# Performance work log

Measured on AMD Instinct MI355X. Metric: run time of the kernel, lower is better.

Reference implementation:

```python
import jax, jax.numpy as jnp
import numpy as np

GT_POSITIVE_THRESHOLD = 3.0  # pixels, from config['gt_positive_threshold']


def setup_inputs() -> dict:
    key = jax.random.key(0)
    k0, k1, k2 = jax.random.split(key, 3)
    B, N0, N1 = 8, 2048, 2048
    W, H = 640.0, 480.0
    scale = jnp.array([W, H], dtype=jnp.float32)
    kpts0 = jax.random.uniform(k0, (B, N0, 2), dtype=jnp.float32) * scale
    kpts1 = jax.random.uniform(k1, (B, N1, 2), dtype=jnp.float32) * scale
    # near-identity homography per pair (small perturbation keeps points in-frame)
    transformation = (jnp.eye(3, dtype=jnp.float32)[None]
                      + 0.001 * jax.random.normal(k2, (B, 3, 3), dtype=jnp.float32))
    return {"kpts0": kpts0, "kpts1": kpts1, "transformation": transformation}


def _reproject_keypoints(kpts, H):
    # kpts: [B,N,2], H: [B,3,3] homography. Homogeneous projection.
    ones = jnp.ones(kpts.shape[:-1] + (1,), dtype=kpts.dtype)
    pts_h = jnp.concatenate([kpts, ones], axis=-1)           # [B,N,3]
    proj = jnp.einsum('bij,bnj->bni', H, pts_h)              # [B,N,3]
    return proj[..., :2] / (proj[..., 2:3] + 1e-8)


def _cdist(a, b):
    # a: [B,N0,2], b: [B,N1,2] -> [B,N0,N1] Euclidean distances
    a2 = jnp.sum(a * a, axis=-1)                             # [B,N0]
    b2 = jnp.sum(b * b, axis=-1)                             # [B,N1]
    ab = jnp.einsum('bnd,bmd->bnm', a, b)                    # [B,N0,N1]
    d2 = a2[:, :, None] + b2[:, None, :] - 2.0 * ab
    return jnp.sqrt(jnp.maximum(d2, 0.0))


def reference(kpts0, kpts1, transformation):
    B, N0, _ = kpts0.shape
    N1 = kpts1.shape[1]
    kpts0_t = _reproject_keypoints(kpts0, transformation)
    err = _cdist(kpts0_t, kpts1)                             # [B,N0,N1]

    min_dist0 = jnp.min(err, axis=2)                         # [B,N0]
    gt_matches0 = jnp.argmin(err, axis=2).astype(jnp.int32)  # [B,N0]
    gt_matches1 = jnp.argmin(err, axis=1).astype(jnp.int32)  # [B,N1]

    # cross-check: kpts1's best match of kpts0's best match must be the kpt itself
    back = jnp.take_along_axis(gt_matches1, gt_matches0, axis=1)  # [B,N0]
    idx0 = jnp.arange(N0, dtype=jnp.int32)[None, :]
    inconsistent = (back != idx0) | (min_dist0 > GT_POSITIVE_THRESHOLD)
    gt_matches0 = jnp.where(inconsistent, -1, gt_matches0)

    # rebuild inverse map: gt_matches1[b, gt_matches0[b,i]] = i for valid i
    valid = gt_matches0 != -1
    tgt = jnp.where(valid, gt_matches0, N1)                  # N1 is out-of-range -> dropped
    src = jnp.broadcast_to(idx0, (B, N0))
    gt_matches1_out = jnp.full((B, N1), -1, dtype=jnp.int32)
    gt_matches1_out = gt_matches1_out.at[jnp.arange(B)[:, None], tgt].set(src, mode='drop')

    return gt_matches0, gt_matches1_out, min_dist0
```

## Files before the change

### kernel.cpp

```cpp
#include <hip/hip_runtime.h>


#define SPN 2048
#define SPT 16384

__device__ __forceinline__ void sp_reproject(const float* __restrict__ T, int b,
                                             float x, float y,
                                             float& X, float& Y, float& S) {
  const float* H = T + b * 9;
  float p0 = __fadd_rn(__fadd_rn(__fmul_rn(H[0], x), __fmul_rn(H[1], y)), H[2]);
  float p1 = __fadd_rn(__fadd_rn(__fmul_rn(H[3], x), __fmul_rn(H[4], y)), H[5]);
  float p2 = __fadd_rn(__fadd_rn(__fmul_rn(H[6], x), __fmul_rn(H[7], y)), H[8]);
  float den = __fadd_rn(p2, 1e-8f);
  X = __fdiv_rn(p0, den);
  Y = __fdiv_rn(p1, den);
  S = __fadd_rn(__fmul_rn(X, X), __fmul_rn(Y, Y));
}

__global__ __launch_bounds__(256) void sp_prep(
    const float2* __restrict__ k0, const float2* __restrict__ k1,
    const float* __restrict__ T, float4* __restrict__ q0, float4* __restrict__ q1) {
  int t = blockIdx.x * 256 + threadIdx.x;
  if (t < SPT) {
    float2 p = k0[t];
    float X, Y, S;
    sp_reproject(T, t >> 11, p.x, p.y, X, Y, S);
    q0[t] = make_float4(X, Y, S, 0.0f);
  } else {
    int u = t - SPT;
    float2 p = k1[u];
    float S = __fadd_rn(__fmul_rn(p.x, p.x), __fmul_rn(p.y, p.y));
    q1[u] = make_float4(p.x, p.y, S, 0.0f);
  }
}

__device__ __forceinline__ void sp_row8(
    const float rx[8], const float ry[8], const float rs[8],
    float bv[8], int bi[8], float4 v, int c) {
#pragma unroll
  for (int r = 0; r < 8; r++) {
    float ab = __fadd_rn(__fmul_rn(rx[r], v.x), __fmul_rn(ry[r], v.y));
    float d2 = __fsub_rn(__fadd_rn(rs[r], v.z), __fmul_rn(2.0f, ab));
    float dm = fmaxf(d2, 0.0f);
    if (dm < bv[r]) { bv[r] = dm; bi[r] = c; }
  }
}

__global__ __launch_bounds__(256, 4) void SuperPointMatchesGenerator_56925496541369_kernel(
    const float4* __restrict__ q0, const float4* __restrict__ q1,
    unsigned short* __restrict__ gt0p, unsigned short* __restrict__ gt1,
    float* __restrict__ out_mind) {
  const bool m1 = blockIdx.x >= SPN;
  const int base = (m1 ? blockIdx.x - SPN : blockIdx.x) * 8;
  const int b = base >> 11, cb = b << 11;
  const float4* __restrict__ qr = m1 ? q1 : q0;
  const float4* __restrict__ qc = (m1 ? q0 : q1) + cb;

  float rx[8], ry[8], rs[8], bv[8];
  int bi[8];
#pragma unroll
  for (int r = 0; r < 8; r++) {
    float4 v = qr[base + r];
    rx[r] = v.x; ry[r] = v.y; rs[r] = v.z;
    bv[r] = INFINITY; bi[r] = 0;
  }

#pragma unroll 1
  for (int c = threadIdx.x; c < SPN; c += 512) {
    float4 va = qc[c];
    float4 vb = qc[c + 256];
    sp_row8(rx, ry, rs, bv, bi, va, c);
    sp_row8(rx, ry, rs, bv, bi, vb, c + 256);
  }

  unsigned long long key[8];
#pragma unroll
  for (int r = 0; r < 8; r++)
    key[r] = ((unsigned long long)__float_as_uint(bv[r]) << 32) | (unsigned)bi[r];
#pragma unroll
  for (int off = 32; off > 0; off >>= 1) {
#pragma unroll
    for (int r = 0; r < 8; r++) {
      unsigned long long o = __shfl_down(key[r], off);
      if (o < key[r]) key[r] = o;
    }
  }
  __shared__ unsigned long long part[4][8];
  if ((threadIdx.x & 63) == 0) {
    int w = threadIdx.x >> 6;
#pragma unroll
    for (int r = 0; r < 8; r++) part[w][r] = key[r];
  }
  __syncthreads();
  if (threadIdx.x < 8) {
    int r = threadIdx.x;
    unsigned long long k = part[0][r];
#pragma unroll
    for (int w = 1; w < 4; w++)
      if (part[w][r] < k) k = part[w][r];
    int idx = (int)(k & 0x7ffu);
    if (!m1) {
      float e = __fsqrt_rn(__uint_as_float((unsigned)(k >> 32)));
      unsigned short pk = (unsigned short)idx;
      if (e > 3.0f) pk |= 0x8000u;
      gt0p[base + r] = pk;
      out_mind[base + r] = e;
    } else {
      gt1[base + r] = (unsigned short)idx;
    }
  }
}

__global__ __launch_bounds__(256) void SuperPointMatchesGenerator_56925496541369_final(
    const unsigned short* __restrict__ gt0p, const unsigned short* __restrict__ gt1,
    float* __restrict__ out) {
  int t = blockIdx.x * 256 + threadIdx.x;
  if (t >= SPT) return;
  int b = t >> 11, i = t & 2047, cb = b << 11;

  unsigned short p0 = gt0p[t];
  int m0 = p0 & 0x7ff;
  bool ok0 = ((p0 & 0x8000u) == 0) && ((int)gt1[cb + m0] == i);
  out[t] = ok0 ? (float)m0 : -1.0f;

  int istar = gt1[t];
  unsigned short ps = gt0p[cb + istar];
  bool ok1 = (((int)(ps & 0x7ff)) == i) && ((ps & 0x8000u) == 0);
  out[SPT + t] = ok1 ? (float)istar : -1.0f;
}

__global__ __launch_bounds__(256) void sp_fb_main(
    const float2* __restrict__ k0, const float2* __restrict__ k1,
    const float* __restrict__ T, unsigned short* __restrict__ gt0p,
    unsigned short* __restrict__ gt1, float* __restrict__ out_mind) {
  const bool mode1 = blockIdx.x >= SPN;
  const int base = (mode1 ? blockIdx.x - SPN : blockIdx.x) * 8;
  const int b = base >> 11, cb = b << 11;
  float rx[8], ry[8], rs[8], bv[8];
  int bi[8];
#pragma unroll
  for (int r = 0; r < 8; r++) { bv[r] = INFINITY; bi[r] = 0; }
  if (!mode1) {
#pragma unroll
    for (int r = 0; r < 8; r++) {
      float2 p = k0[base + r];
      sp_reproject(T, b, p.x, p.y, rx[r], ry[r], rs[r]);
    }
    for (int c = threadIdx.x; c < SPN; c += 256) {
      float2 p = k1[cb + c];
      float b2 = __fadd_rn(__fmul_rn(p.x, p.x), __fmul_rn(p.y, p.y));
#pragma unroll
      for (int r = 0; r < 8; r++) {
        float ab = __fadd_rn(__fmul_rn(rx[r], p.x), __fmul_rn(ry[r], p.y));
        float d2 = __fsub_rn(__fadd_rn(rs[r], b2), __fmul_rn(2.0f, ab));
        float dm = fmaxf(d2, 0.0f);
        if (dm < bv[r]) { bv[r] = dm; bi[r] = c; }
      }
    }
  } else {
#pragma unroll
    for (int r = 0; r < 8; r++) {
      float2 p = k1[base + r];
      rx[r] = p.x; ry[r] = p.y;
      rs[r] = __fadd_rn(__fmul_rn(p.x, p.x), __fmul_rn(p.y, p.y));
    }
    for (int c = threadIdx.x; c < SPN; c += 256) {
      float2 p = k0[cb + c];
      float cx, cy, a2;
      sp_reproject(T, b, p.x, p.y, cx, cy, a2);
#pragma unroll
      for (int r = 0; r < 8; r++) {
        float ab = __fadd_rn(__fmul_rn(rx[r], cx), __fmul_rn(ry[r], cy));
        float d2 = __fsub_rn(__fadd_rn(a2, rs[r]), __fmul_rn(2.0f, ab));
        float dm = fmaxf(d2, 0.0f);
        if (dm < bv[r]) { bv[r] = dm; bi[r] = c; }
      }
    }
  }
  unsigned long long key[8];
#pragma unroll
  for (int r = 0; r < 8; r++)
    key[r] = ((unsigned long long)__float_as_uint(bv[r]) << 32) | (unsigned)bi[r];
#pragma unroll
  for (int off = 32; off > 0; off >>= 1) {
#pragma unroll
    for (int r = 0; r < 8; r++) {
      unsigned long long o = __shfl_down(key[r], off);
      if (o < key[r]) key[r] = o;
    }
  }
  __shared__ unsigned long long part[4][8];
  if ((threadIdx.x & 63) == 0) {
    int w = threadIdx.x >> 6;
#pragma unroll
    for (int r = 0; r < 8; r++) part[w][r] = key[r];
  }
  __syncthreads();
  if (threadIdx.x < 8) {
    int r = threadIdx.x;
    unsigned long long k = part[0][r];
#pragma unroll
    for (int w = 1; w < 4; w++)
      if (part[w][r] < k) k = part[w][r];
    int idx = (int)(k & 0x7ffu);
    if (!mode1) {
      float e = __fsqrt_rn(__uint_as_float((unsigned)(k >> 32)));
      unsigned short pk = (unsigned short)idx;
      if (e > 3.0f) pk |= 0x8000u;
      gt0p[base + r] = pk;
      out_mind[base + r] = e;
    } else {
      gt1[base + r] = (unsigned short)idx;
    }
  }
}

extern "C" void kernel_launch(void* const* d_in, const int* in_sizes, int n_in,
                              void* d_out, int out_size, void* d_ws, size_t ws_size,
                              hipStream_t stream) {
  (void)in_sizes; (void)n_in; (void)out_size;
  const float2* k0 = (const float2*)d_in[0];
  const float2* k1 = (const float2*)d_in[1];
  const float* T   = (const float*)d_in[2];
  float* out = (float*)d_out;

  const size_t need = (size_t)2 * SPT * sizeof(float4) + (size_t)2 * SPT * sizeof(unsigned short);
  if (ws_size >= need) {
    float4* q0 = (float4*)d_ws;
    float4* q1 = q0 + SPT;
    unsigned short* gt0p = (unsigned short*)(q1 + SPT);
    unsigned short* gt1  = gt0p + SPT;
    sp_prep<<<2 * SPT / 256, 256, 0, stream>>>(k0, k1, T, q0, q1);
    SuperPointMatchesGenerator_56925496541369_kernel<<<2 * SPN, 256, 0, stream>>>(
        q0, q1, gt0p, gt1, out + 2 * SPT);
    SuperPointMatchesGenerator_56925496541369_final<<<SPT / 256, 256, 0, stream>>>(
        gt0p, gt1, out);
  } else {
    unsigned short* gt0p = (unsigned short*)d_ws;
    unsigned short* gt1  = gt0p + SPT;
    sp_fb_main<<<2 * SPN, 256, 0, stream>>>(k0, k1, T, gt0p, gt1, out + 2 * SPT);
    SuperPointMatchesGenerator_56925496541369_final<<<SPT / 256, 256, 0, stream>>>(
        gt0p, gt1, out);
  }
}
```

Measured before the change: 82.36 us.

## Stage candidates in LDS, process 16 rows per block, reduce via shared memory

Each block now loads the batch's 2048 candidate points into a 32KB shared-memory tile and tracks 16 rows per thread instead of 8, halving the block count. The clamp to zero moves after the loop, and the doubled row coordinates are precomputed to shave arithmetic per pair. The final argmin reduction goes through shared memory, with each wave finishing four rows. This trades extra LDS use and register pressure (lower occupancy) for less global traffic and more reuse per candidate load.

```diff
diff --git a/kernel.cpp b/kernel.cpp
--- a/kernel.cpp
+++ b/kernel.cpp
@@ -34,79 +34,84 @@
   }
 }
 
-__device__ __forceinline__ void sp_row8(
-    const float rx[8], const float ry[8], const float rs[8],
-    float bv[8], int bi[8], float4 v, int c) {
-#pragma unroll
-  for (int r = 0; r < 8; r++) {
-    float ab = __fadd_rn(__fmul_rn(rx[r], v.x), __fmul_rn(ry[r], v.y));
-    float d2 = __fsub_rn(__fadd_rn(rs[r], v.z), __fmul_rn(2.0f, ab));
-    float dm = fmaxf(d2, 0.0f);
-    if (dm < bv[r]) { bv[r] = dm; bi[r] = c; }
-  }
-}
-
 __global__ __launch_bounds__(256, 4) void SuperPointMatchesGenerator_56925496541369_kernel(
     const float4* __restrict__ q0, const float4* __restrict__ q1,
     unsigned short* __restrict__ gt0p, unsigned short* __restrict__ gt1,
     float* __restrict__ out_mind) {
-  const bool m1 = blockIdx.x >= SPN;
-  const int base = (m1 ? blockIdx.x - SPN : blockIdx.x) * 8;
+  __shared__ float4 cand[SPN];
+  const int tid = threadIdx.x;
+  const bool m1 = blockIdx.x >= (SPT / 16);
+  const int base = (m1 ? blockIdx.x - (SPT / 16) : blockIdx.x) << 4;
   const int b = base >> 11, cb = b << 11;
   const float4* __restrict__ qr = m1 ? q1 : q0;
   const float4* __restrict__ qc = (m1 ? q0 : q1) + cb;
 
-  float rx[8], ry[8], rs[8], bv[8];
-  int bi[8];
-#pragma unroll
-  for (int r = 0; r < 8; r++) {
+  float4 stage[8];
+#pragma unroll
+  for (int k = 0; k < 8; k++) stage[k] = qc[(k << 8) + tid];
+#pragma unroll
+  for (int k = 0; k < 8; k++) cand[(k << 8) + tid] = stage[k];
+
+  float rx2[16], ry2[16], rsv[16], bv[16];
+  int bi[16];
+#pragma unroll
+  for (int r = 0; r < 16; r++) {
     float4 v = qr[base + r];
-    rx[r] = v.x; ry[r] = v.y; rs[r] = v.z;
+    rx2[r] = __fmul_rn(2.0f, v.x);
+    ry2[r] = __fmul_rn(2.0f, v.y);
+    rsv[r] = v.z;
     bv[r] = INFINITY; bi[r] = 0;
   }
-
-#pragma unroll 1
-  for (int c = threadIdx.x; c < SPN; c += 512) {
-    float4 va = qc[c];
-    float4 vb = qc[c + 256];
-    sp_row8(rx, ry, rs, bv, bi, va, c);
-    sp_row8(rx, ry, rs, bv, bi, vb, c + 256);
-  }
-
-  unsigned long long key[8];
-#pragma unroll
-  for (int r = 0; r < 8; r++)
-    key[r] = ((unsigned long long)__float_as_uint(bv[r]) << 32) | (unsigned)bi[r];
-#pragma unroll
-  for (int off = 32; off > 0; off >>= 1) {
-#pragma unroll
-    for (int r = 0; r < 8; r++) {
-      unsigned long long o = __shfl_down(key[r], off);
-      if (o < key[r]) key[r] = o;
-    }
-  }
-  __shared__ unsigned long long part[4][8];
-  if ((threadIdx.x & 63) == 0) {
-    int w = threadIdx.x >> 6;
-#pragma unroll
-    for (int r = 0; r < 8; r++) part[w][r] = key[r];
-  }
-  __syncthreads();
-  if (threadIdx.x < 8) {
-    int r = threadIdx.x;
-    unsigned long long k = part[0][r];
-#pragma unroll
-    for (int w = 1; w < 4; w++)
-      if (part[w][r] < k) k = part[w][r];
-    int idx = (int)(k & 0x7ffu);
-    if (!m1) {
-      float e = __fsqrt_rn(__uint_as_float((unsigned)(k >> 32)));
-      unsigned short pk = (unsigned short)idx;
-      if (e > 3.0f) pk |= 0x8000u;
-      gt0p[base + r] = pk;
-      out_mind[base + r] = e;
-    } else {
-      gt1[base + r] = (unsigned short)idx;
+  __syncthreads();
+
+#pragma unroll 2
+  for (int k = 0; k < 8; k++) {
+    const int c = (k << 8) + tid;
+    float4 v = cand[c];
+#pragma unroll
+    for (int r = 0; r < 16; r++) {
+      float tw = __fadd_rn(__fmul_rn(rx2[r], v.x), __fmul_rn(ry2[r], v.y));
+      float s  = __fadd_rn(rsv[r], v.z);
+      float d2 = __fsub_rn(s, tw);
+      if (d2 < bv[r]) { bv[r] = d2; bi[r] = c; }
+    }
+  }
+  __syncthreads();
+
+  unsigned long long* keys = (unsigned long long*)cand;
+#pragma unroll
+  for (int r = 0; r < 16; r++) {
+    float dm = fmaxf(bv[r], 0.0f);
+    keys[(r << 8) + tid] =
+        ((unsigned long long)__float_as_uint(dm) << 32) | (unsigned)bi[r];
+  }
+  __syncthreads();
+
+  const int wv = tid >> 6, ln = tid & 63;
+#pragma unroll
+  for (int rr = 0; rr < 4; rr++) {
+    const int r = (wv << 2) + rr;
+    unsigned long long k0 = keys[(r << 8) + ln];
+    unsigned long long t;
+    t = keys[(r << 8) + 64 + ln];  if (t < k0) k0 = t;
+    t = keys[(r << 8) + 128 + ln]; if (t < k0) k0 = t;
+    t = keys[(r << 8) + 192 + ln]; if (t < k0) k0 = t;
+#pragma unroll
+    for (int off = 32; off > 0; off >>= 1) {
+      unsigned long long o = __shfl_down(k0, off);
+      if (o < k0) k0 = o;
+    }
+    if (ln == 0) {
+      int idx = (int)(k0 & 0x7ffu);
+      if (!m1) {
+        float e = __fsqrt_rn(__uint_as_float((unsigned)(k0 >> 32)));
+        unsigned short pk = (unsigned short)idx;
+        if (e > 3.0f) pk |= 0x8000u;
+        gt0p[base + r] = pk;
+        out_mind[base + r] = e;
+      } else {
+        gt1[base + r] = (unsigned short)idx;
+      }
     }
   }
 }
@@ -231,7 +236,7 @@
     unsigned short* gt0p = (unsigned short*)(q1 + SPT);
     unsigned short* gt1  = gt0p + SPT;
     sp_prep<<<2 * SPT / 256, 256, 0, stream>>>(k0, k1, T, q0, q1);
-    SuperPointMatchesGenerator_56925496541369_kernel<<<2 * SPN, 256, 0, stream>>>(
+    SuperPointMatchesGenerator_56925496541369_kernel<<<2 * (SPT / 16), 256, 0, stream>>>(
         q0, q1, gt0p, gt1, out + 2 * SPT);
     SuperPointMatchesGenerator_56925496541369_final<<<SPT / 256, 256, 0, stream>>>(
         gt0p, gt1, out);
```

Result: no change. 81.44 us (-1.1%).
